# Performance work log

Measured on AMD Instinct MI355X. Metric: run time of the kernel, lower is better.

The kernel has to match this reference:

```python
import jax, jax.numpy as jnp
import numpy as np

B, L, TAGSET = 512, 1024, 50
T = TAGSET + 2          # tagset_size + 2 (START, STOP)
START = T - 2           # START_TAG = -2
STOP = T - 1            # STOP_TAG = -1


def setup_inputs() -> dict:
    key = jax.random.key(0)
    k1, k2, k3, k4 = jax.random.split(key, 4)
    feats = jax.random.normal(k1, (B, L, T), jnp.float32)
    transitions = jax.random.normal(k2, (T, T), jnp.float32) * 0.1
    lengths = jax.random.randint(k3, (B,), L // 2, L + 1)
    mask = jnp.arange(L)[None, :] < lengths[:, None]          # (B, L) bool, prefix mask
    tags = jax.random.randint(k4, (B, L), 0, TAGSET)          # gold tags in [0, tagset_size)
    return {"feats": feats, "transitions": transitions, "mask": mask, "tags": tags}


def _crf_nll(feats, transitions, mask, tags):
    # feats: (B, L, T) float; transitions: (T, T); mask: (B, L) bool; tags: (B, L) int
    Bx = feats.shape[0]
    f = jnp.swapaxes(feats, 0, 1)   # (L, B, T)
    m = jnp.swapaxes(mask, 0, 1)    # (L, B)

    # ---- forward algorithm (log partition) ----
    # scores[t, b, i, j] = feats[t, b, j] + transitions[i, j]
    # init: partition = scores[0][:, START, :]
    part0 = f[0] + transitions[START][None, :]                # (B, T)

    def step(part, xs):
        ft, mt = xs                                           # (B, T), (B,)
        cur = ft[:, None, :] + transitions[None, :, :] + part[:, :, None]  # (B, T, T)
        new = jax.scipy.special.logsumexp(cur, axis=1)        # (B, T)
        part = jnp.where(mt[:, None], new, part)              # masked update
        return part, None

    part, _ = jax.lax.scan(step, part0, (f[1:], m[1:]))
    final = jax.scipy.special.logsumexp(transitions[None, :, :] + part[:, :, None], axis=1)
    forward_score = final[:, STOP].sum()

    # ---- gold sequence score ----
    emit = jnp.take_along_axis(feats, tags[..., None], axis=-1)[..., 0]   # (B, L)
    prev = jnp.concatenate([jnp.full((Bx, 1), START, dtype=tags.dtype), tags[:, :-1]], axis=1)
    trans_sc = transitions[prev, tags]                                    # (B, L)
    lengths = mask.sum(axis=1).astype(jnp.int32)
    end_ids = jnp.take_along_axis(tags, (lengths - 1)[:, None], axis=1)[:, 0]
    gold_score = jnp.sum((emit + trans_sc) * mask) + transitions[end_ids, STOP].sum()

    # average_batch = True
    return (forward_score - gold_score) / Bx


def reference(feats, transitions, mask, tags):
    return _crf_nll(feats, transitions, mask, tags)
```

## Files before the change

### kernel.cpp

```cpp
#include <hip/hip_runtime.h>

#define BB 512
#define LL 1024
#define TT 52
#define START_TAG 50
#define STOP_TAG  51

__device__ __forceinline__ float rl(float v, int i) {
  return __uint_as_float(__builtin_amdgcn_readlane(__float_as_uint(v), (unsigned)i));
}
__device__ __forceinline__ float wave_max(float v) {
#pragma unroll
  for (int off = 32; off; off >>= 1) v = fmaxf(v, __shfl_xor(v, off, 64));
  return v;
}
__device__ __forceinline__ float wave_sum(float v) {
#pragma unroll
  for (int off = 32; off; off >>= 1) v += __shfl_xor(v, off, 64);
  return v;
}
__device__ __forceinline__ int wave_sum_i(int v) {
#pragma unroll
  for (int off = 32; off; off >>= 1) v += __shfl_xor(v, off, 64);
  return v;
}

#define EGROUPS(G)                                                      \
  G(0, 1, 2, 3) G(4, 5, 6, 7) G(8, 9, 10, 11) G(12, 13, 14, 15)        \
  G(16, 17, 18, 19) G(20, 21, 22, 23) G(24, 25, 26, 27)                \
  G(28, 29, 30, 31) G(32, 33, 34, 35) G(36, 37, 38, 39)                \
  G(40, 41, 42, 43) G(44, 45, 46, 47) G(48, 49, 50, 51)

__global__ __launch_bounds__(64)
__attribute__((amdgpu_waves_per_eu(1, 1)))
void crf_main(
    const float* __restrict__ feats, const float* __restrict__ trans,
    const void* __restrict__ maskp, const int* __restrict__ tags,
    float* __restrict__ res) {
  const int b = blockIdx.x;
  const int lane = threadIdx.x;
  const bool jok = lane < TT;
  const int j = jok ? lane : TT - 1;

  const unsigned* m32 = (const unsigned*)maskp;
  int s = 0;
  const unsigned v0 = m32[0];
  if (v0 == 0x01010101u) {
    const uint4* mv = (const uint4*)maskp;
    uint4 x = mv[b * 64 + lane];
    s  = (int)(((x.x & 0x01010101u) * 0x01010101u) >> 24);
    s += (int)(((x.y & 0x01010101u) * 0x01010101u) >> 24);
    s += (int)(((x.z & 0x01010101u) * 0x01010101u) >> 24);
    s += (int)(((x.w & 0x01010101u) * 0x01010101u) >> 24);
  } else if (m32[1] == 0u) {
    const unsigned long long* m64 = (const unsigned long long*)maskp;
#pragma unroll
    for (int k = 0; k < 16; ++k) s += (int)m64[(size_t)b * LL + k * 64 + lane];
  } else {
    const int* mi = (const int*)maskp;
#pragma unroll
    for (int k = 0; k < 16; ++k) s += mi[b * LL + k * 64 + lane];
  }
  const int len = wave_sum_i(s);

#define EDECL(a, b_, c, d)                                   \
  float E##a  = jok ? __expf(trans[(a)*TT + j]) : 0.f;       \
  float E##b_ = jok ? __expf(trans[(b_)*TT + j]) : 0.f;      \
  float E##c  = jok ? __expf(trans[(c)*TT + j]) : 0.f;       \
  float E##d  = jok ? __expf(trans[(d)*TT + j]) : 0.f;
  EGROUPS(EDECL)

  const float tl = jok ? __expf(trans[j * TT + STOP_TAG]) : 0.f;

  const float* fp = feats + (size_t)b * LL * TT + j;
  float p = __expf(fp[0]) * E50;
  float carry2 = 0.f;

#define RLDECL(a, b_, c, d)                 \
  const float P##a  = rl(p, (a));           \
  const float P##b_ = rl(p, (b_));          \
  const float P##c  = rl(p, (c));           \
  const float P##d  = rl(p, (d));
#define EFMA(a, b_, c, d)                   \
  a0 = fmaf(P##a, E##a, a0);                \
  a1 = fmaf(P##b_, E##b_, a1);              \
  a2 = fmaf(P##c, E##c, a2);                \
  a3 = fmaf(P##d, E##d, a3);

#define CRF_STEP(FV)                        \
  {                                         \
    const float eft = __expf((FV)-6.0f);    \
    EGROUPS(RLDECL)                         \
    __builtin_amdgcn_sched_barrier(0);      \
    float a0 = 0.f, a1 = 0.f, a2 = 0.f, a3 = 0.f; \
    EGROUPS(EFMA)                           \
    p = ((a0 + a1) + (a2 + a3)) * eft;      \
  }

#define EPIN(a, b_, c, d) \
  asm volatile("" : "+v"(E##a), "+v"(E##b_), "+v"(E##c), "+v"(E##d));

#define CH 16
  const int nsteps = len - 1;
  const int nchunk = nsteps / CH;
  const int ntail = nsteps % CH;

  float fb[CH];
#pragma unroll
  for (int k = 0; k < CH; ++k) fb[k] = fp[(size_t)(1 + k) * TT];

  int tbase = 1;
  for (int c = 0; c < nchunk; ++c) {
    EGROUPS(EPIN)
    float fn[CH];
#pragma unroll
    for (int k = 0; k < CH; ++k) {
      int tt = tbase + CH + k;
      tt = tt < len ? tt : len - 1;
      fn[k] = fp[(size_t)tt * TT];
    }
#pragma unroll
    for (int k = 0; k < CH; ++k) CRF_STEP(fb[k]);
    const float m = wave_max(p);
    carry2 += __log2f(m);
    p *= __builtin_amdgcn_rcpf(m);
#pragma unroll
    for (int k = 0; k < CH; ++k) fb[k] = fn[k];
    tbase += CH;
  }
#pragma unroll
  for (int k = 0; k < CH; ++k)
    if (k < ntail) CRF_STEP(fb[k]);

  const float sfin = wave_sum(p * tl);
  const float fwd =
      (__log2f(sfin) + carry2) * 0.6931471805599453f + 6.0f * (float)(len - 1);

  const int* tgb = tags + b * LL;
  float g = 0.f;
  for (int base = 0; base < len; base += 64) {
    const int t = base + lane;
    if (t < len) {
      const int tag = tgb[t];
      const int prev = (t == 0) ? START_TAG : tgb[t - 1];
      g += feats[((size_t)b * LL + t) * TT + tag] + trans[prev * TT + tag];
    }
  }
  g = wave_sum(g);

  if (lane == 0) {
    g += trans[tgb[len - 1] * TT + STOP_TAG];
    res[b] = fwd - g;
  }
#undef CRF_STEP
#undef EFMA
#undef RLDECL
#undef ESTEP4
#undef EDECL
#undef EPIN
}

__global__ __launch_bounds__(64) void crf_fin(const float* __restrict__ res,
                                              float* __restrict__ out) {
  float s = 0.f;
#pragma unroll
  for (int k = 0; k < 8; ++k) s += res[threadIdx.x + k * 64];
  s = wave_sum(s);
  if (threadIdx.x == 0) out[0] = s * (1.0f / (float)BB);
}

extern "C" void kernel_launch(void* const* d_in, const int* in_sizes, int n_in,
                              void* d_out, int out_size, void* d_ws, size_t ws_size,
                              hipStream_t stream) {
  const float* feats = (const float*)d_in[0];
  const float* trans = (const float*)d_in[1];
  const void* mask   = (const void*)d_in[2];
  const int* tags    = (const int*)d_in[3];

  float* res = (float*)d_ws;

  crf_main<<<BB, 64, 0, stream>>>(feats, trans, mask, tags, res);
  crf_fin<<<1, 64, 0, stream>>>(res, (float*)d_out);
}
```

Baseline: 355.3 us.

## Split CRF forward recurrence across four waves with LDS reduction per step

Each batch row now runs on four waves. Each wave holds 13 of the 52 transition rows and computes a partial sum over its source tags, and the partials are combined through double-buffered shared memory with a barrier every timestep. This shortens the serial readlane/FMA chain per step by about four times. In exchange it adds an LDS write, an s_barrier and an LDS read on the critical path of every one of up to 1023 sequential steps. The block is now four times larger, so fewer batches fit per CU.

```diff
diff --git a/kernel.cpp b/kernel.cpp
--- a/kernel.cpp
+++ b/kernel.cpp
@@ -5,6 +5,9 @@
 #define TT 52
 #define START_TAG 50
 #define STOP_TAG  51
+#define NW 4
+#define IPW 13
+#define CH 16
 
 __device__ __forceinline__ float rl(float v, int i) {
   return __uint_as_float(__builtin_amdgcn_readlane(__float_as_uint(v), (unsigned)i));
@@ -25,22 +28,20 @@
   return v;
 }
 
-#define EGROUPS(G)                                                      \
-  G(0, 1, 2, 3) G(4, 5, 6, 7) G(8, 9, 10, 11) G(12, 13, 14, 15)        \
-  G(16, 17, 18, 19) G(20, 21, 22, 23) G(24, 25, 26, 27)                \
-  G(28, 29, 30, 31) G(32, 33, 34, 35) G(36, 37, 38, 39)                \
-  G(40, 41, 42, 43) G(44, 45, 46, 47) G(48, 49, 50, 51)
-
-__global__ __launch_bounds__(64)
-__attribute__((amdgpu_waves_per_eu(1, 1)))
+__global__ __launch_bounds__(256)
+__attribute__((amdgpu_waves_per_eu(2)))
 void crf_main(
     const float* __restrict__ feats, const float* __restrict__ trans,
     const void* __restrict__ maskp, const int* __restrict__ tags,
     float* __restrict__ res) {
+  __shared__ float xch[2][NW][64];
   const int b = blockIdx.x;
-  const int lane = threadIdx.x;
+  const int tid = threadIdx.x;
+  const int wid = tid >> 6;
+  const int lane = tid & 63;
   const bool jok = lane < TT;
   const int j = jok ? lane : TT - 1;
+  const int wbase = wid * IPW;
 
   const unsigned* m32 = (const unsigned*)maskp;
   int s = 0;
@@ -63,44 +64,45 @@
   }
   const int len = wave_sum_i(s);
 
-#define EDECL(a, b_, c, d)                                   \
-  float E##a  = jok ? __expf(trans[(a)*TT + j]) : 0.f;       \
-  float E##b_ = jok ? __expf(trans[(b_)*TT + j]) : 0.f;      \
-  float E##c  = jok ? __expf(trans[(c)*TT + j]) : 0.f;       \
-  float E##d  = jok ? __expf(trans[(d)*TT + j]) : 0.f;
-  EGROUPS(EDECL)
-
-  const float tl = jok ? __expf(trans[j * TT + STOP_TAG]) : 0.f;
+#define EDECL(k) float E##k = jok ? __expf(trans[(wbase + (k)) * TT + j]) : 0.f;
+  EDECL(0) EDECL(1) EDECL(2) EDECL(3) EDECL(4) EDECL(5) EDECL(6)
+  EDECL(7) EDECL(8) EDECL(9) EDECL(10) EDECL(11) EDECL(12)
+#undef EDECL
 
   const float* fp = feats + (size_t)b * LL * TT + j;
-  float p = __expf(fp[0]) * E50;
+  float p = jok ? __expf(fp[0]) * __expf(trans[START_TAG * TT + j]) : 0.f;
   float carry2 = 0.f;
 
-#define RLDECL(a, b_, c, d)                 \
-  const float P##a  = rl(p, (a));           \
-  const float P##b_ = rl(p, (b_));          \
-  const float P##c  = rl(p, (c));           \
-  const float P##d  = rl(p, (d));
-#define EFMA(a, b_, c, d)                   \
-  a0 = fmaf(P##a, E##a, a0);                \
-  a1 = fmaf(P##b_, E##b_, a1);              \
-  a2 = fmaf(P##c, E##c, a2);                \
-  a3 = fmaf(P##d, E##d, a3);
-
-#define CRF_STEP(FV)                        \
-  {                                         \
-    const float eft = __expf((FV)-6.0f);    \
-    EGROUPS(RLDECL)                         \
-    __builtin_amdgcn_sched_barrier(0);      \
-    float a0 = 0.f, a1 = 0.f, a2 = 0.f, a3 = 0.f; \
-    EGROUPS(EFMA)                           \
-    p = ((a0 + a1) + (a2 + a3)) * eft;      \
+#define CRF_STEP(FV, PAR)                                                \
+  {                                                                      \
+    const float eft = __expf((FV)-6.0f);                                 \
+    const float P0 = rl(p, wbase + 0),  P1 = rl(p, wbase + 1);           \
+    const float P2 = rl(p, wbase + 2),  P3 = rl(p, wbase + 3);           \
+    const float P4 = rl(p, wbase + 4),  P5 = rl(p, wbase + 5);           \
+    const float P6 = rl(p, wbase + 6),  P7 = rl(p, wbase + 7);           \
+    const float P8 = rl(p, wbase + 8),  P9 = rl(p, wbase + 9);           \
+    const float P10 = rl(p, wbase + 10), P11 = rl(p, wbase + 11);        \
+    const float P12 = rl(p, wbase + 12);                                 \
+    __builtin_amdgcn_sched_barrier(0);                                   \
+    float a0 = P0 * E0, a1 = P1 * E1, a2 = P2 * E2, a3 = P3 * E3;        \
+    a0 = fmaf(P4, E4, a0); a1 = fmaf(P5, E5, a1);                        \
+    a2 = fmaf(P6, E6, a2); a3 = fmaf(P7, E7, a3);                        \
+    a0 = fmaf(P8, E8, a0); a1 = fmaf(P9, E9, a1);                        \
+    a2 = fmaf(P10, E10, a2); a3 = fmaf(P11, E11, a3);                    \
+    a0 = fmaf(P12, E12, a0);                                             \
+    xch[PAR][wid][lane] = (a0 + a1) + (a2 + a3);                         \
+    asm volatile("s_waitcnt lgkmcnt(0)" ::: "memory");                   \
+    __builtin_amdgcn_s_barrier();                                        \
+    const float r0 = xch[PAR][0][lane], r1 = xch[PAR][1][lane];          \
+    const float r2 = xch[PAR][2][lane], r3 = xch[PAR][3][lane];          \
+    p = ((r0 + r1) + (r2 + r3)) * eft;                                   \
   }
 
-#define EPIN(a, b_, c, d) \
-  asm volatile("" : "+v"(E##a), "+v"(E##b_), "+v"(E##c), "+v"(E##d));
+#define EPIN                                                             \
+  asm volatile("" : "+v"(E0), "+v"(E1), "+v"(E2), "+v"(E3), "+v"(E4),    \
+                    "+v"(E5), "+v"(E6), "+v"(E7), "+v"(E8), "+v"(E9),    \
+                    "+v"(E10), "+v"(E11), "+v"(E12));
 
-#define CH 16
   const int nsteps = len - 1;
   const int nchunk = nsteps / CH;
   const int ntail = nsteps % CH;
@@ -111,7 +113,7 @@
 
   int tbase = 1;
   for (int c = 0; c < nchunk; ++c) {
-    EGROUPS(EPIN)
+    EPIN
     float fn[CH];
 #pragma unroll
     for (int k = 0; k < CH; ++k) {
@@ -120,7 +122,7 @@
       fn[k] = fp[(size_t)tt * TT];
     }
 #pragma unroll
-    for (int k = 0; k < CH; ++k) CRF_STEP(fb[k]);
+    for (int k = 0; k < CH; ++k) CRF_STEP(fb[k], ((k + 1) & 1));
     const float m = wave_max(p);
     carry2 += __log2f(m);
     p *= __builtin_amdgcn_rcpf(m);
@@ -130,33 +132,32 @@
   }
 #pragma unroll
   for (int k = 0; k < CH; ++k)
-    if (k < ntail) CRF_STEP(fb[k]);
+    if (k < ntail) CRF_STEP(fb[k], ((k + 1) & 1));
 
-  const float sfin = wave_sum(p * tl);
-  const float fwd =
-      (__log2f(sfin) + carry2) * 0.6931471805599453f + 6.0f * (float)(len - 1);
+  if (wid == 0) {
+    const float tl = jok ? __expf(trans[j * TT + STOP_TAG]) : 0.f;
+    const float sfin = wave_sum(p * tl);
+    const float fwd =
+        (__log2f(sfin) + carry2) * 0.6931471805599453f + 6.0f * (float)(len - 1);
 
-  const int* tgb = tags + b * LL;
-  float g = 0.f;
-  for (int base = 0; base < len; base += 64) {
-    const int t = base + lane;
-    if (t < len) {
-      const int tag = tgb[t];
-      const int prev = (t == 0) ? START_TAG : tgb[t - 1];
-      g += feats[((size_t)b * LL + t) * TT + tag] + trans[prev * TT + tag];
+    const int* tgb = tags + b * LL;
+    float g = 0.f;
+    for (int base = 0; base < len; base += 64) {
+      const int t = base + lane;
+      if (t < len) {
+        const int tag = tgb[t];
+        const int prev = (t == 0) ? START_TAG : tgb[t - 1];
+        g += feats[((size_t)b * LL + t) * TT + tag] + trans[prev * TT + tag];
+      }
+    }
+    g = wave_sum(g);
+
+    if (lane == 0) {
+      g += trans[tgb[len - 1] * TT + STOP_TAG];
+      res[b] = fwd - g;
     }
   }
-  g = wave_sum(g);
-
-  if (lane == 0) {
-    g += trans[tgb[len - 1] * TT + STOP_TAG];
-    res[b] = fwd - g;
-  }
 #undef CRF_STEP
-#undef EFMA
-#undef RLDECL
-#undef ESTEP4
-#undef EDECL
 #undef EPIN
 }
 
@@ -179,6 +180,6 @@
 
   float* res = (float*)d_ws;
 
-  crf_main<<<BB, 64, 0, stream>>>(feats, trans, mask, tags, res);
+  crf_main<<<BB, NW * 64, 0, stream>>>(feats, trans, mask, tags, res);
   crf_fin<<<1, 64, 0, stream>>>(res, (float*)d_out);
 }
```

Result: slower. 410.3 us (+15.5%).

## Broadcast forward-recursion state via LDS and use packed FMA for transitions

Applied to the files above, without the earlier changes.

Each forward step previously pulled every one of the 52 partition values out of its lane with a separate v_readlane before doing 52 scalar FMAs. Now each lane writes its value to a small shared-memory vector. Every lane then reads it back as thirteen 128-bit broadcast loads and accumulates with 26 v_pk_fma_f32 ops against transition exponentials stored as float pairs. This aims to cut the per-step broadcast and FMA instruction count on the serial recurrence, at the cost of an LDS write-then-read round trip and longer dependent accumulator chains on every step.

```diff
diff --git a/kernel.cpp b/kernel.cpp
--- a/kernel.cpp
+++ b/kernel.cpp
@@ -5,10 +5,15 @@
 #define TT 52
 #define START_TAG 50
 #define STOP_TAG  51
+#define CH 16
 
-__device__ __forceinline__ float rl(float v, int i) {
-  return __uint_as_float(__builtin_amdgcn_readlane(__float_as_uint(v), (unsigned)i));
+typedef __attribute__((ext_vector_type(2))) float f32x2;
+typedef __attribute__((ext_vector_type(4))) float f32x4;
+
+__device__ __forceinline__ void pkfma(f32x2& acc, f32x2 a, f32x2 b) {
+  asm("v_pk_fma_f32 %0, %1, %2, %0" : "+v"(acc) : "v"(a), "v"(b));
 }
+
 __device__ __forceinline__ float wave_max(float v) {
 #pragma unroll
   for (int off = 32; off; off >>= 1) v = fmaxf(v, __shfl_xor(v, off, 64));
@@ -25,18 +30,13 @@
   return v;
 }
 
-#define EGROUPS(G)                                                      \
-  G(0, 1, 2, 3) G(4, 5, 6, 7) G(8, 9, 10, 11) G(12, 13, 14, 15)        \
-  G(16, 17, 18, 19) G(20, 21, 22, 23) G(24, 25, 26, 27)                \
-  G(28, 29, 30, 31) G(32, 33, 34, 35) G(36, 37, 38, 39)                \
-  G(40, 41, 42, 43) G(44, 45, 46, 47) G(48, 49, 50, 51)
-
 __global__ __launch_bounds__(64)
 __attribute__((amdgpu_waves_per_eu(1, 1)))
 void crf_main(
     const float* __restrict__ feats, const float* __restrict__ trans,
     const void* __restrict__ maskp, const int* __restrict__ tags,
     float* __restrict__ res) {
+  __shared__ __align__(16) float pvec[64];
   const int b = blockIdx.x;
   const int lane = threadIdx.x;
   const bool jok = lane < TT;
@@ -63,44 +63,37 @@
   }
   const int len = wave_sum_i(s);
 
-#define EDECL(a, b_, c, d)                                   \
-  float E##a  = jok ? __expf(trans[(a)*TT + j]) : 0.f;       \
-  float E##b_ = jok ? __expf(trans[(b_)*TT + j]) : 0.f;      \
-  float E##c  = jok ? __expf(trans[(c)*TT + j]) : 0.f;       \
-  float E##d  = jok ? __expf(trans[(d)*TT + j]) : 0.f;
-  EGROUPS(EDECL)
-
-  const float tl = jok ? __expf(trans[j * TT + STOP_TAG]) : 0.f;
+  f32x2 Ek[26];
+#pragma unroll
+  for (int m = 0; m < 26; ++m) {
+    const float e0 = jok ? __expf(trans[(2 * m) * TT + j]) : 0.f;
+    const float e1 = jok ? __expf(trans[(2 * m + 1) * TT + j]) : 0.f;
+    Ek[m].x = e0;
+    Ek[m].y = e1;
+  }
 
   const float* fp = feats + (size_t)b * LL * TT + j;
-  float p = __expf(fp[0]) * E50;
+  float p = __expf(fp[0]) * Ek[25].x;
   float carry2 = 0.f;
 
-#define RLDECL(a, b_, c, d)                 \
-  const float P##a  = rl(p, (a));           \
-  const float P##b_ = rl(p, (b_));          \
-  const float P##c  = rl(p, (c));           \
-  const float P##d  = rl(p, (d));
-#define EFMA(a, b_, c, d)                   \
-  a0 = fmaf(P##a, E##a, a0);                \
-  a1 = fmaf(P##b_, E##b_, a1);              \
-  a2 = fmaf(P##c, E##c, a2);                \
-  a3 = fmaf(P##d, E##d, a3);
-
-#define CRF_STEP(FV)                        \
-  {                                         \
-    const float eft = __expf((FV)-6.0f);    \
-    EGROUPS(RLDECL)                         \
-    __builtin_amdgcn_sched_barrier(0);      \
-    float a0 = 0.f, a1 = 0.f, a2 = 0.f, a3 = 0.f; \
-    EGROUPS(EFMA)                           \
-    p = ((a0 + a1) + (a2 + a3)) * eft;      \
+#define CRF_STEP(FV)                                                     \
+  {                                                                      \
+    const float eft = __expf((FV)-6.0f);                                 \
+    pvec[lane] = p;                                                      \
+    f32x2 aA = {0.f, 0.f}, aB = {0.f, 0.f};                              \
+    _Pragma("unroll") for (int m = 0; m < 13; ++m) {                     \
+      const f32x4 P4 = *(const f32x4*)&pvec[4 * m];                      \
+      pkfma(aA, __builtin_shufflevector(P4, P4, 0, 1), Ek[2 * m]);       \
+      pkfma(aB, __builtin_shufflevector(P4, P4, 2, 3), Ek[2 * m + 1]);   \
+    }                                                                    \
+    const f32x2 aS = aA + aB;                                            \
+    p = (aS.x + aS.y) * eft;                                             \
   }
 
-#define EPIN(a, b_, c, d) \
-  asm volatile("" : "+v"(E##a), "+v"(E##b_), "+v"(E##c), "+v"(E##d));
+#define EPIN                                                             \
+  _Pragma("unroll") for (int m = 0; m < 26; ++m)                         \
+      asm volatile("" : "+v"(Ek[m]));
 
-#define CH 16
   const int nsteps = len - 1;
   const int nchunk = nsteps / CH;
   const int ntail = nsteps % CH;
@@ -111,7 +104,7 @@
 
   int tbase = 1;
   for (int c = 0; c < nchunk; ++c) {
-    EGROUPS(EPIN)
+    EPIN
     float fn[CH];
 #pragma unroll
     for (int k = 0; k < CH; ++k) {
@@ -132,6 +125,7 @@
   for (int k = 0; k < CH; ++k)
     if (k < ntail) CRF_STEP(fb[k]);
 
+  const float tl = jok ? __expf(trans[j * TT + STOP_TAG]) : 0.f;
   const float sfin = wave_sum(p * tl);
   const float fwd =
       (__log2f(sfin) + carry2) * 0.6931471805599453f + 6.0f * (float)(len - 1);
@@ -153,10 +147,6 @@
     res[b] = fwd - g;
   }
 #undef CRF_STEP
-#undef EFMA
-#undef RLDECL
-#undef ESTEP4
-#undef EDECL
 #undef EPIN
 }
 
```

Result: no change. 360.0 us (+1.3%).
